# Performance work log

Hardware: AMD Instinct MI355X
Metric: run time of the kernel (lower is better)

The kernel has to match this reference:

```python
import jax, jax.numpy as jnp
import numpy as np


def setup_inputs() -> dict:
    key = jax.random.key(0)
    k1, k2 = jax.random.split(key)
    B, M, QT, KVT, H = 4, 16, 1024, 1024, 64
    s = jax.random.normal(k1, (B, M, QT, KVT), dtype=jnp.float32)
    v = jax.random.normal(k2, (B, M, KVT, H), dtype=jnp.float32)
    return {"s": s, "v": v}


def reference(s, v):
    # Original: broadcast-multiply [B,M,QT,KVT,H] then sum over KVT.
    # Mathematically a batched matmul: out[b,m,q,h] = sum_k s[b,m,q,k] * v[b,m,k,h]
    return jnp.einsum('bmqk,bmkh->bmqh', s, v)
```

## Files before the change

kernel.cpp:

```cpp
#include <hip/hip_runtime.h>
#include <stdint.h>


typedef __bf16 bf16x8 __attribute__((ext_vector_type(8)));
typedef float  f32x4  __attribute__((ext_vector_type(4)));

#define QTDIM 1024
#define KVDIM 1024
#define HDIM  64
#define QTILE 64
#define BK    64
#define NK    (KVDIM / BK)
#define SSTR  72
#define THREADS 256

__device__ __forceinline__ uint32_t pack_bf16_2(float lo, float hi) {
    union { float f; uint32_t u; } a, b;
    a.f = lo; b.f = hi;
    return __builtin_amdgcn_perm(b.u, a.u, 0x07060302u);
}

__global__ __launch_bounds__(THREADS, 4) void svbmm_kernel(
    const float* __restrict__ s, const float* __restrict__ v, float* __restrict__ out)
{
    __shared__ uint16_t s_sm[2][QTILE * SSTR];
    __shared__ uint16_t vt_sm[2][HDIM * SSTR];

    const int tid = threadIdx.x;
    const int bm  = blockIdx.y;
    const int q0  = blockIdx.x * QTILE;

    const float* sp = s   + ((size_t)bm * QTDIM + q0) * (size_t)KVDIM;
    const float* vp = v   + (size_t)bm * KVDIM * HDIM;
    float*       op = out + ((size_t)bm * QTDIM + q0) * (size_t)HDIM;

    const int srow = tid >> 4;
    const int scol = (tid & 15) << 2;
    const int vh   = tid & 63;
    const int vk0  = (tid >> 6) << 4;

    float4 sreg[4];
    float  vreg[16];

    {
        const float* sb = sp + srow * KVDIM + scol;
        #pragma unroll
        for (int i = 0; i < 4; ++i)
            sreg[i] = *(const float4*)(sb + i * 16 * KVDIM);
        const float* vb = vp + vk0 * HDIM + vh;
        #pragma unroll
        for (int j = 0; j < 16; ++j)
            vreg[j] = vb[j * HDIM];
    }

    f32x4 acc[4];
    #pragma unroll
    for (int nt = 0; nt < 4; ++nt)
        acc[nt] = (f32x4){0.f, 0.f, 0.f, 0.f};

    const int wave = tid >> 6;
    const int lane = tid & 63;
    const int lrow = lane & 15;
    const int quad = lane >> 4;

    #pragma unroll 2
    for (int kt = 0; kt < NK; ++kt) {
        const int buf = kt & 1;

        #pragma unroll
        for (int i = 0; i < 4; ++i) {
            float4 f = sreg[i];
            uint64_t u = (uint64_t)pack_bf16_2(f.x, f.y)
                       | ((uint64_t)pack_bf16_2(f.z, f.w) << 32);
            *(uint64_t*)&s_sm[buf][(srow + i * 16) * SSTR + scol] = u;
        }
        #pragma unroll
        for (int p = 0; p < 4; ++p) {
            uint64_t u = (uint64_t)pack_bf16_2(vreg[4 * p],     vreg[4 * p + 1])
                       | ((uint64_t)pack_bf16_2(vreg[4 * p + 2], vreg[4 * p + 3]) << 32);
            *(uint64_t*)&vt_sm[buf][vh * SSTR + vk0 + 4 * p] = u;
        }

        __syncthreads();

        if (kt + 1 < NK) {
            const float* sb = sp + srow * KVDIM + (kt + 1) * BK + scol;
            #pragma unroll
            for (int i = 0; i < 4; ++i)
                sreg[i] = *(const float4*)(sb + i * 16 * KVDIM);
            const float* vb = vp + ((kt + 1) * BK + vk0) * HDIM + vh;
            #pragma unroll
            for (int j = 0; j < 16; ++j)
                vreg[j] = vb[j * HDIM];
        }

        #pragma unroll
        for (int kk = 0; kk < 2; ++kk) {
            const int col = kk * 32 + quad * 8;
            bf16x8 a = *(const bf16x8*)&s_sm[buf][(wave * 16 + lrow) * SSTR + col];
            #pragma unroll
            for (int nt = 0; nt < 4; ++nt) {
                bf16x8 b = *(const bf16x8*)&vt_sm[buf][(nt * 16 + lrow) * SSTR + col];
                acc[nt] = __builtin_amdgcn_mfma_f32_16x16x32_bf16(a, b, acc[nt], 0, 0, 0);
            }
        }
    }

    #pragma unroll
    for (int nt = 0; nt < 4; ++nt) {
        #pragma unroll
        for (int r = 0; r < 4; ++r) {
            const int row = wave * 16 + quad * 4 + r;
            const int col = nt * 16 + lrow;
            op[row * HDIM + col] = acc[nt][r];
        }
    }
}

extern "C" void kernel_launch(void* const* d_in, const int* in_sizes, int n_in,
                              void* d_out, int out_size, void* d_ws, size_t ws_size,
                              hipStream_t stream) {
    const float* s = (const float*)d_in[0];
    const float* v = (const float*)d_in[1];
    float* out = (float*)d_out;
    const int BM = in_sizes[0] / (QTDIM * KVDIM);
    dim3 grid(QTDIM / QTILE, BM);
    svbmm_kernel<<<grid, THREADS, 0, stream>>>(s, v, out);
}
```

Before: 380.9 us.

## Pre-pack V into MFMA fragment layout and stream operands directly from global memory

Adds a prepass kernel that transposes V, converts it to bf16 and writes it to workspace in the exact per-lane MFMA B-fragment order. The main kernel drops shared memory and barriers. Each wave loads its S rows as float4 straight from global memory, converts them in registers, and register-double-buffers both operands. This removes LDS staging and sync overhead, but each of the 4 waves in a block now rereads the packed V from global/L2, and the prepass adds an extra launch.

```diff
diff --git a/kernel.cpp b/kernel.cpp
--- a/kernel.cpp
+++ b/kernel.cpp
@@ -2,16 +2,15 @@
 #include <stdint.h>
 
 
-typedef __bf16 bf16x8 __attribute__((ext_vector_type(8)));
-typedef float  f32x4  __attribute__((ext_vector_type(4)));
+typedef __bf16    bf16x8 __attribute__((ext_vector_type(8)));
+typedef float     f32x4  __attribute__((ext_vector_type(4)));
+typedef uint32_t  u32x4  __attribute__((ext_vector_type(4)));
 
 #define QTDIM 1024
 #define KVDIM 1024
 #define HDIM  64
 #define QTILE 64
-#define BK    64
-#define NK    (KVDIM / BK)
-#define SSTR  72
+#define NKS   (KVDIM / 32)
 #define THREADS 256
 
 __device__ __forceinline__ uint32_t pack_bf16_2(float lo, float hi) {
@@ -20,99 +19,117 @@
     return __builtin_amdgcn_perm(b.u, a.u, 0x07060302u);
 }
 
-__global__ __launch_bounds__(THREADS, 4) void svbmm_kernel(
-    const float* __restrict__ s, const float* __restrict__ v, float* __restrict__ out)
+__device__ __forceinline__ bf16x8 as_bf16x8(u32x4 u) {
+    union { u32x4 u; bf16x8 b; } c; c.u = u; return c.b;
+}
+
+__global__ __launch_bounds__(256) void vtrans_kernel(
+    const float* __restrict__ v, uint16_t* __restrict__ vtf)
 {
-    __shared__ uint16_t s_sm[2][QTILE * SSTR];
-    __shared__ uint16_t vt_sm[2][HDIM * SSTR];
+    __shared__ float lds[64][68];
 
     const int tid = threadIdx.x;
+    const int kb  = blockIdx.x;
     const int bm  = blockIdx.y;
-    const int q0  = blockIdx.x * QTILE;
 
-    const float* sp = s   + ((size_t)bm * QTDIM + q0) * (size_t)KVDIM;
-    const float* vp = v   + (size_t)bm * KVDIM * HDIM;
-    float*       op = out + ((size_t)bm * QTDIM + q0) * (size_t)HDIM;
+    const float* vp = v + ((size_t)bm * KVDIM + (size_t)kb * 64) * HDIM;
 
-    const int srow = tid >> 4;
-    const int scol = (tid & 15) << 2;
-    const int vh   = tid & 63;
-    const int vk0  = (tid >> 6) << 4;
+    #pragma unroll
+    for (int i = 0; i < 4; ++i) {
+        int f = i * 256 + tid;
+        int r = f >> 4, c4 = f & 15;
+        float4 val = *(const float4*)(vp + r * HDIM + c4 * 4);
+        *(float4*)&lds[r][c4 * 4] = val;
+    }
+    __syncthreads();
 
-    float4 sreg[4];
-    float  vreg[16];
+    const int lane = tid & 63;
+    const int w    = tid >> 6;
+    const int lrow = lane & 15;
+    const int quad = lane >> 4;
+    const int col  = w * 16 + lrow;
 
-    {
-        const float* sb = sp + srow * KVDIM + scol;
-        #pragma unroll
-        for (int i = 0; i < 4; ++i)
-            sreg[i] = *(const float4*)(sb + i * 16 * KVDIM);
-        const float* vb = vp + vk0 * HDIM + vh;
-        #pragma unroll
-        for (int j = 0; j < 16; ++j)
-            vreg[j] = vb[j * HDIM];
+    #pragma unroll
+    for (int t = 0; t < 2; ++t) {
+        const int ks   = kb * 2 + t;
+        const int kloc = t * 32 + quad * 8;
+        u32x4 pk;
+        pk.x = pack_bf16_2(lds[kloc + 0][col], lds[kloc + 1][col]);
+        pk.y = pack_bf16_2(lds[kloc + 2][col], lds[kloc + 3][col]);
+        pk.z = pack_bf16_2(lds[kloc + 4][col], lds[kloc + 5][col]);
+        pk.w = pack_bf16_2(lds[kloc + 6][col], lds[kloc + 7][col]);
+        size_t off = ((((size_t)bm * 32 + ks) * 4 + w) * 64 + lane) * 8;
+        *(u32x4*)&vtf[off] = pk;
     }
+}
+
+__global__ __launch_bounds__(THREADS, 4) void svbmm_kernel(
+    const float* __restrict__ s, const uint16_t* __restrict__ vtf,
+    float* __restrict__ out)
+{
+    const int tid  = threadIdx.x;
+    const int bm   = blockIdx.y;
+    const int q0   = blockIdx.x * QTILE;
+    const int wave = tid >> 6;
+    const int lane = tid & 63;
+    const int lrow = lane & 15;
+    const int quad = lane >> 4;
+
+    const float* __restrict__ sp =
+        s + ((size_t)bm * QTDIM + q0 + wave * 16 + lrow) * KVDIM + quad * 8;
+    const uint16_t* __restrict__ vp =
+        vtf + ((size_t)bm * 32 * 4 * 64 + lane) * 8;
 
     f32x4 acc[4];
     #pragma unroll
     for (int nt = 0; nt < 4; ++nt)
         acc[nt] = (f32x4){0.f, 0.f, 0.f, 0.f};
 
-    const int wave = tid >> 6;
-    const int lane = tid & 63;
-    const int lrow = lane & 15;
-    const int quad = lane >> 4;
+    auto step = [&](float4 f0, float4 f1, u32x4 b0, u32x4 b1, u32x4 b2, u32x4 b3) {
+        u32x4 au;
+        au.x = pack_bf16_2(f0.x, f0.y);
+        au.y = pack_bf16_2(f0.z, f0.w);
+        au.z = pack_bf16_2(f1.x, f1.y);
+        au.w = pack_bf16_2(f1.z, f1.w);
+        bf16x8 a = as_bf16x8(au);
+        acc[0] = __builtin_amdgcn_mfma_f32_16x16x32_bf16(a, as_bf16x8(b0), acc[0], 0, 0, 0);
+        acc[1] = __builtin_amdgcn_mfma_f32_16x16x32_bf16(a, as_bf16x8(b1), acc[1], 0, 0, 0);
+        acc[2] = __builtin_amdgcn_mfma_f32_16x16x32_bf16(a, as_bf16x8(b2), acc[2], 0, 0, 0);
+        acc[3] = __builtin_amdgcn_mfma_f32_16x16x32_bf16(a, as_bf16x8(b3), acc[3], 0, 0, 0);
+    };
 
-    #pragma unroll 2
-    for (int kt = 0; kt < NK; ++kt) {
-        const int buf = kt & 1;
+    float4 pa0 = *(const float4*)(sp);
+    float4 pa1 = *(const float4*)(sp + 4);
+    u32x4  pb0 = *(const u32x4*)(vp);
+    u32x4  pb1 = *(const u32x4*)(vp + 512);
+    u32x4  pb2 = *(const u32x4*)(vp + 1024);
+    u32x4  pb3 = *(const u32x4*)(vp + 1536);
 
-        #pragma unroll
-        for (int i = 0; i < 4; ++i) {
-            float4 f = sreg[i];
-            uint64_t u = (uint64_t)pack_bf16_2(f.x, f.y)
-                       | ((uint64_t)pack_bf16_2(f.z, f.w) << 32);
-            *(uint64_t*)&s_sm[buf][(srow + i * 16) * SSTR + scol] = u;
-        }
-        #pragma unroll
-        for (int p = 0; p < 4; ++p) {
-            uint64_t u = (uint64_t)pack_bf16_2(vreg[4 * p],     vreg[4 * p + 1])
-                       | ((uint64_t)pack_bf16_2(vreg[4 * p + 2], vreg[4 * p + 3]) << 32);
-            *(uint64_t*)&vt_sm[buf][vh * SSTR + vk0 + 4 * p] = u;
-        }
+    #pragma unroll 4
+    for (int ks = 0; ks < NKS - 1; ++ks) {
+        const float*    sn = sp + (size_t)(ks + 1) * 32;
+        const uint16_t* vn = vp + (size_t)(ks + 1) * 2048;
 
-        __syncthreads();
+        float4 ca0 = pa0, ca1 = pa1;
+        u32x4  cb0 = pb0, cb1 = pb1, cb2 = pb2, cb3 = pb3;
 
-        if (kt + 1 < NK) {
-            const float* sb = sp + srow * KVDIM + (kt + 1) * BK + scol;
-            #pragma unroll
-            for (int i = 0; i < 4; ++i)
-                sreg[i] = *(const float4*)(sb + i * 16 * KVDIM);
-            const float* vb = vp + ((kt + 1) * BK + vk0) * HDIM + vh;
-            #pragma unroll
-            for (int j = 0; j < 16; ++j)
-                vreg[j] = vb[j * HDIM];
-        }
+        pa0 = *(const float4*)(sn);
+        pa1 = *(const float4*)(sn + 4);
+        pb0 = *(const u32x4*)(vn);
+        pb1 = *(const u32x4*)(vn + 512);
+        pb2 = *(const u32x4*)(vn + 1024);
+        pb3 = *(const u32x4*)(vn + 1536);
 
-        #pragma unroll
-        for (int kk = 0; kk < 2; ++kk) {
-            const int col = kk * 32 + quad * 8;
-            bf16x8 a = *(const bf16x8*)&s_sm[buf][(wave * 16 + lrow) * SSTR + col];
-            #pragma unroll
-            for (int nt = 0; nt < 4; ++nt) {
-                bf16x8 b = *(const bf16x8*)&vt_sm[buf][(nt * 16 + lrow) * SSTR + col];
-                acc[nt] = __builtin_amdgcn_mfma_f32_16x16x32_bf16(a, b, acc[nt], 0, 0, 0);
-            }
-        }
+        step(ca0, ca1, cb0, cb1, cb2, cb3);
     }
+    step(pa0, pa1, pb0, pb1, pb2, pb3);
 
+    float* __restrict__ op = out + ((size_t)bm * QTDIM + q0 + wave * 16) * HDIM;
     #pragma unroll
     for (int nt = 0; nt < 4; ++nt) {
         #pragma unroll
         for (int r = 0; r < 4; ++r) {
-            const int row = wave * 16 + quad * 4 + r;
-            const int col = nt * 16 + lrow;
-            op[row * HDIM + col] = acc[nt][r];
+            op[(quad * 4 + r) * HDIM + nt * 16 + lrow] = acc[nt][r];
         }
     }
 }
@@ -124,6 +141,12 @@
     const float* v = (const float*)d_in[1];
     float* out = (float*)d_out;
     const int BM = in_sizes[0] / (QTDIM * KVDIM);
+
+    uint16_t* vtf = (uint16_t*)d_ws;
+
+    dim3 gridT(KVDIM / 64, BM);
+    vtrans_kernel<<<gridT, 256, 0, stream>>>(v, vtf);
+
     dim3 grid(QTDIM / QTILE, BM);
-    svbmm_kernel<<<grid, THREADS, 0, stream>>>(s, v, out);
+    svbmm_kernel<<<grid, THREADS, 0, stream>>>(s, vtf, out);
 }
```

Measured after the change: 403.6 us. 1.06x slower.

## Pre-pack V into MFMA fragment layout in a separate bf16 transpose kernel

Applied to the files above, without the earlier changes.

Adds a pre-pass kernel that converts V to bf16 and stores it in the exact per-lane MFMA B-operand order in workspace. The main kernel then loads B fragments straight from global memory into registers, removing the V shared-memory staging, its per-tile packing work and the strided fp32 V loads. This costs an extra kernel launch and a workspace round trip, and the loads are issued after the barrier, so their latency is exposed inside the loop rather than prefetched.

```diff
diff --git a/kernel.cpp b/kernel.cpp
--- a/kernel.cpp
+++ b/kernel.cpp
@@ -2,8 +2,9 @@
 #include <stdint.h>
 
 
-typedef __bf16 bf16x8 __attribute__((ext_vector_type(8)));
-typedef float  f32x4  __attribute__((ext_vector_type(4)));
+typedef __bf16    bf16x8 __attribute__((ext_vector_type(8)));
+typedef float     f32x4  __attribute__((ext_vector_type(4)));
+typedef uint32_t  u32x4  __attribute__((ext_vector_type(4)));
 
 #define QTDIM 1024
 #define KVDIM 1024
@@ -20,37 +21,60 @@
     return __builtin_amdgcn_perm(b.u, a.u, 0x07060302u);
 }
 
+__device__ __forceinline__ bf16x8 as_bf16x8(u32x4 u) {
+    union { u32x4 u; bf16x8 b; } c; c.u = u; return c.b;
+}
+
+__global__ __launch_bounds__(256) void vtrans_kernel(
+    const float* __restrict__ v, uint16_t* __restrict__ vtf)
+{
+    const int tid  = threadIdx.x;
+    const int lane = tid & 63;
+    const int w    = tid >> 6;
+    const int ks   = blockIdx.x;
+    const int bm   = blockIdx.y;
+    const int lrow = lane & 15;
+    const int quad = lane >> 4;
+
+    const float* vp = v + ((size_t)bm * KVDIM + ks * 32 + quad * 8) * HDIM
+                        + w * 16 + lrow;
+    float f[8];
+    #pragma unroll
+    for (int j = 0; j < 8; ++j) f[j] = vp[j * HDIM];
+
+    u32x4 pk;
+    pk.x = pack_bf16_2(f[0], f[1]);
+    pk.y = pack_bf16_2(f[2], f[3]);
+    pk.z = pack_bf16_2(f[4], f[5]);
+    pk.w = pack_bf16_2(f[6], f[7]);
+
+    size_t off = ((((size_t)bm * 32 + ks) * 4 + w) * 64 + lane) * 8;
+    *(u32x4*)&vtf[off] = pk;
+}
+
 __global__ __launch_bounds__(THREADS, 4) void svbmm_kernel(
-    const float* __restrict__ s, const float* __restrict__ v, float* __restrict__ out)
+    const float* __restrict__ s, const uint16_t* __restrict__ vtf,
+    float* __restrict__ out)
 {
     __shared__ uint16_t s_sm[2][QTILE * SSTR];
-    __shared__ uint16_t vt_sm[2][HDIM * SSTR];
 
     const int tid = threadIdx.x;
     const int bm  = blockIdx.y;
     const int q0  = blockIdx.x * QTILE;
 
     const float* sp = s   + ((size_t)bm * QTDIM + q0) * (size_t)KVDIM;
-    const float* vp = v   + (size_t)bm * KVDIM * HDIM;
     float*       op = out + ((size_t)bm * QTDIM + q0) * (size_t)HDIM;
 
     const int srow = tid >> 4;
     const int scol = (tid & 15) << 2;
-    const int vh   = tid & 63;
-    const int vk0  = (tid >> 6) << 4;
 
     float4 sreg[4];
-    float  vreg[16];
 
     {
         const float* sb = sp + srow * KVDIM + scol;
         #pragma unroll
         for (int i = 0; i < 4; ++i)
             sreg[i] = *(const float4*)(sb + i * 16 * KVDIM);
-        const float* vb = vp + vk0 * HDIM + vh;
-        #pragma unroll
-        for (int j = 0; j < 16; ++j)
-            vreg[j] = vb[j * HDIM];
     }
 
     f32x4 acc[4];
@@ -63,6 +87,8 @@
     const int lrow = lane & 15;
     const int quad = lane >> 4;
 
+    const uint16_t* vp = vtf + ((size_t)bm * 32 * 4 * 64 + (size_t)lane) * 8;
+
     #pragma unroll 2
     for (int kt = 0; kt < NK; ++kt) {
         const int buf = kt & 1;
@@ -74,24 +100,23 @@
                        | ((uint64_t)pack_bf16_2(f.z, f.w) << 32);
             *(uint64_t*)&s_sm[buf][(srow + i * 16) * SSTR + scol] = u;
         }
-        #pragma unroll
-        for (int p = 0; p < 4; ++p) {
-            uint64_t u = (uint64_t)pack_bf16_2(vreg[4 * p],     vreg[4 * p + 1])
-                       | ((uint64_t)pack_bf16_2(vreg[4 * p + 2], vreg[4 * p + 3]) << 32);
-            *(uint64_t*)&vt_sm[buf][vh * SSTR + vk0 + 4 * p] = u;
-        }
 
         __syncthreads();
 
+        u32x4 b[8];
+        {
+            const uint16_t* vb = vp + (size_t)kt * 4096;
+            #pragma unroll
+            for (int kk = 0; kk < 2; ++kk)
+                #pragma unroll
+                for (int nt = 0; nt < 4; ++nt)
+                    b[kk * 4 + nt] = *(const u32x4*)(vb + kk * 2048 + nt * 512);
+        }
         if (kt + 1 < NK) {
             const float* sb = sp + srow * KVDIM + (kt + 1) * BK + scol;
             #pragma unroll
             for (int i = 0; i < 4; ++i)
                 sreg[i] = *(const float4*)(sb + i * 16 * KVDIM);
-            const float* vb = vp + ((kt + 1) * BK + vk0) * HDIM + vh;
-            #pragma unroll
-            for (int j = 0; j < 16; ++j)
-                vreg[j] = vb[j * HDIM];
         }
 
         #pragma unroll
@@ -99,10 +124,9 @@
             const int col = kk * 32 + quad * 8;
             bf16x8 a = *(const bf16x8*)&s_sm[buf][(wave * 16 + lrow) * SSTR + col];
             #pragma unroll
-            for (int nt = 0; nt < 4; ++nt) {
-                bf16x8 b = *(const bf16x8*)&vt_sm[buf][(nt * 16 + lrow) * SSTR + col];
-                acc[nt] = __builtin_amdgcn_mfma_f32_16x16x32_bf16(a, b, acc[nt], 0, 0, 0);
-            }
+            for (int nt = 0; nt < 4; ++nt)
+                acc[nt] = __builtin_amdgcn_mfma_f32_16x16x32_bf16(
+                    a, as_bf16x8(b[kk * 4 + nt]), acc[nt], 0, 0, 0);
         }
     }
 
@@ -124,6 +148,12 @@
     const float* v = (const float*)d_in[1];
     float* out = (float*)d_out;
     const int BM = in_sizes[0] / (QTDIM * KVDIM);
+
+    uint16_t* vtf = (uint16_t*)d_ws;
+
+    dim3 gridT(KVDIM / 32, BM);
+    vtrans_kernel<<<gridT, 256, 0, stream>>>(v, vtf);
+
     dim3 grid(QTDIM / QTILE, BM);
-    svbmm_kernel<<<grid, THREADS, 0, stream>>>(s, v, out);
+    svbmm_kernel<<<grid, THREADS, 0, stream>>>(s, vtf, out);
 }
```

New measurement: 395.3 us. 3.8% more time.
